# Performance work log

Hardware: AMD Instinct MI355X
Metric: run time of the kernel (lower is better)

## Reference

```python
import jax, jax.numpy as jnp
import numpy as np

N = 4096          # nodes
IN_DIM = 256
OUT_DIM = 128
EDGE_DIM = 64
N_SAMPLE = 128
N_EDGES = 65536   # undirected edges (edge ids 1..N_EDGES; id 0 = no edge)
ALPHA = 0.2       # leaky-relu negative slope


def _glorot(key, shape):
    fan_in, fan_out = shape[0], shape[-1]
    scale = 1.414 * np.sqrt(2.0 / (fan_in + fan_out))
    return jax.random.normal(key, shape, jnp.float32) * scale


def setup_inputs() -> dict:
    rng = np.random.default_rng(0)
    # sample unique undirected edges (i < j); np.unique sorts lexicographically,
    # which matches torch's row-major e_index.nonzero() ordering, so assigning
    # sequential ids 1..n here makes edges == arange(1, n+1) in the update step.
    ii = rng.integers(0, N, size=3 * N_EDGES)
    jj = rng.integers(0, N, size=3 * N_EDGES)
    lo, hi = np.minimum(ii, jj), np.maximum(ii, jj)
    ok = lo < hi
    pairs = np.unique(np.stack([lo[ok], hi[ok]], axis=1), axis=0)[:N_EDGES]
    n = pairs.shape[0]
    ids = np.arange(1, n + 1, dtype=np.int32)
    e_index = np.zeros((N, N), np.int32)
    e_index[pairs[:, 0], pairs[:, 1]] = ids
    e_index[pairs[:, 1], pairs[:, 0]] = ids
    # per-node neighbor sampling with replacement (hoisted from torch forward)
    neigh = np.empty((N, N_SAMPLE), np.int32)
    for v in range(N):
        nz = np.nonzero(e_index[v])[0]
        neigh[v] = v if nz.size == 0 else rng.choice(nz, N_SAMPLE)

    key = jax.random.key(0)
    ks = jax.random.split(key, 8)
    return {
        "features": jax.random.normal(ks[0], (N, IN_DIM), jnp.float32),
        "e_index": jnp.asarray(e_index),
        "neigh": jnp.asarray(neigh),
        "to_update": jnp.asarray(pairs.astype(np.int32)),
        "emb": jax.random.normal(ks[1], (n + 1, EDGE_DIM), jnp.float32),
        "W": _glorot(ks[2], (IN_DIM, OUT_DIM)),
        "W2": _glorot(ks[3], (OUT_DIM, EDGE_DIM)),
        "W3": _glorot(ks[4], (EDGE_DIM, EDGE_DIM)),
        "B": _glorot(ks[5], (1, EDGE_DIM)),
        "a": _glorot(ks[6], (2 * OUT_DIM + EDGE_DIM, 1)),
    }


def reference(features, e_index, neigh, to_update, emb, W, W2, W3, B, a):
    x = features @ W                                        # [N, OUT]
    xn = x[neigh]                                           # [N, S, OUT] gather
    eid = jnp.take_along_axis(e_index, neigh, axis=1)       # [N, S] edge ids
    en = emb[eid]                                           # [N, S, ED] gather
    a_input = jnp.concatenate(
        [jnp.broadcast_to(x[:, None, :], xn.shape), xn, en], axis=2
    )                                                       # [N, S, 2*OUT+ED]
    e = jax.nn.leaky_relu((a_input @ a)[..., 0], ALPHA)     # [N, S]
    att = jax.nn.softmax(e, axis=1)                         # dropout = id (eval)
    h_prime = jnp.einsum('ns,nsd->nd', att, xn)             # [N, OUT]
    output = jax.nn.elu(h_prime + x)
    # edge update: (output[i] + output[j]) @ W2 == matmul(output[pair], W2).sum(1)
    edges = e_index[to_update[:, 0], to_update[:, 1]]       # == 1..n
    v_input = (output[to_update[:, 0]] + output[to_update[:, 1]]) @ W2
    e_input = emb[edges] @ W3
    a_in2 = jnp.concatenate([B, e_input + v_input + B], axis=0)  # [n+1, ED]
    emb_new = jax.nn.relu(a_in2 * emb)
    return output, emb_new
```

## Files before the change

kernel.cpp:

```cpp
#include <hip/hip_runtime.h>
#include <hip/hip_bf16.h>

#define N_NODES 4096
#define IN_DIM  256
#define OUT_DIM 128
#define EDGE_DIM 64
#define N_SAMPLE 128

__device__ __forceinline__ float wsum64(float v) {
#pragma unroll
  for (int off = 32; off; off >>= 1) v += __shfl_xor(v, off, 64);
  return v;
}
__device__ __forceinline__ float sum16(float v) {
#pragma unroll
  for (int off = 1; off < 16; off <<= 1) v += __shfl_xor(v, off, 64);
  return v;
}
__device__ __forceinline__ float bfu(ushort u) {
  return __uint_as_float((unsigned int)u << 16);
}

__global__ void __launch_bounds__(128) k1_kernel(const float* __restrict__ feat,
                                                 const float* __restrict__ W,
                                                 const float* __restrict__ emb,
                                                 const int* __restrict__ eidx,
                                                 const int* __restrict__ neigh,
                                                 const float* __restrict__ a,
                                                 ushort* __restrict__ xh,
                                                 float* __restrict__ s1,
                                                 float* __restrict__ s2,
                                                 float* __restrict__ s3,
                                                 int* __restrict__ eid_vs, int rows) {
  const int t  = threadIdx.x;
  const int v0 = blockIdx.x * 4;
  __shared__ float f[4][IN_DIM];
  __shared__ float redA[8], redB[8];

  int uq[4];
#pragma unroll
  for (int q = 0; q < 4; ++q) uq[q] = neigh[(v0 + q) * N_SAMPLE + t];

  {
    float4* f4 = reinterpret_cast<float4*>(&f[0][0]);
    const float4* g4 = reinterpret_cast<const float4*>(&feat[v0 * IN_DIM]);
    f4[t]       = g4[t];
    f4[t + 128] = g4[t + 128];
  }
  __syncthreads();

  int eq[4];
#pragma unroll
  for (int q = 0; q < 4; ++q) eq[q] = eidx[(v0 + q) * N_NODES + uq[q]];

  float acc[4] = {0.f, 0.f, 0.f, 0.f};
#pragma unroll 2
  for (int i = 0; i < IN_DIM; i += 4) {
    const float w0 = W[(i + 0) * OUT_DIM + t];
    const float w1 = W[(i + 1) * OUT_DIM + t];
    const float w2 = W[(i + 2) * OUT_DIM + t];
    const float w3 = W[(i + 3) * OUT_DIM + t];
#pragma unroll
    for (int r = 0; r < 4; ++r) {
      const float4 fv = *reinterpret_cast<const float4*>(&f[r][i]);
      acc[r] += fv.x * w0 + fv.y * w1 + fv.z * w2 + fv.w * w3;
    }
  }

#pragma unroll
  for (int q = 0; q < 4; ++q) eid_vs[(v0 + q) * N_SAMPLE + t] = eq[q];

  const int wv = t >> 6;
  const float a1t = a[t], a2t = a[OUT_DIM + t];
#pragma unroll
  for (int r = 0; r < 4; ++r) {
    unsigned int ub = __float_as_uint(acc[r]);
    ub += 0x7FFFu + ((ub >> 16) & 1u);
    xh[(v0 + r) * OUT_DIM + t] = (ushort)(ub >> 16);
    const float q1 = wsum64(acc[r] * a1t);
    const float q2 = wsum64(acc[r] * a2t);
    if ((t & 63) == 0) { redA[wv * 4 + r] = q1; redB[wv * 4 + r] = q2; }
  }
  __syncthreads();
  if (t < 4) {
    s1[v0 + t] = redA[t] + redA[4 + t];
    s2[v0 + t] = redB[t] + redB[4 + t];
  }

  const int gw  = blockIdx.x * 2 + wv;
  const int l   = t & 63;
  const int sub = l >> 4, q16 = l & 15;
  const float4 a3q = *reinterpret_cast<const float4*>(&a[2 * OUT_DIM + q16 * 4]);
  for (int r0 = gw * 4; r0 < rows; r0 += 8192) {
    const int r = r0 + sub;
    float v = 0.f;
    if (r < rows) {
      const float4 e4 = *reinterpret_cast<const float4*>(&emb[r * EDGE_DIM + q16 * 4]);
      v = e4.x * a3q.x + e4.y * a3q.y + e4.z * a3q.z + e4.w * a3q.w;
    }
    v = sum16(v);
    if (q16 == 0 && r < rows) s3[r] = v;
  }
}

__global__ void __launch_bounds__(256, 4) k2_attn_y_kernel(const ushort* __restrict__ xh,
                                                           const float* __restrict__ s1,
                                                           const float* __restrict__ s2,
                                                           const float* __restrict__ s3,
                                                           const int* __restrict__ neigh,
                                                           const int* __restrict__ eid_vs,
                                                           const float* __restrict__ W2,
                                                           float* __restrict__ out,
                                                           float* __restrict__ Y) {
  const int v = blockIdx.x;
  const int t = threadIdx.x;
  const int w = t >> 6, l = t & 63;
  __shared__ float attC[N_SAMPLE];
  __shared__ float redC[2];
  __shared__ float4 hpC[8][32];
  __shared__ float orow[OUT_DIM];
  __shared__ float partY[4][EDGE_DIM];

  const int half = l >> 5, cq = l & 31;
  const int s0 = w * 32;
  ushort4 xr[16];
#pragma unroll
  for (int it = 0; it < 16; ++it) {
    const int u = neigh[v * N_SAMPLE + s0 + 2 * it + half];
    xr[it] = *reinterpret_cast<const ushort4*>(&xh[u * OUT_DIM + cq * 4]);
  }

  if (t < N_SAMPLE) {
    const int u   = neigh[v * N_SAMPLE + t];
    const int eid = eid_vs[v * N_SAMPLE + t];
    float e = s1[v] + s2[u] + s3[eid];
    e = e > 0.f ? e : 0.2f * e;
    const float p = __expf(e);
    attC[t] = p;
    const float s = wsum64(p);
    if (l == 0) redC[w] = s;
  }
  __syncthreads();
  const float inv = 1.0f / (redC[0] + redC[1]);

  {
    float4 h4 = make_float4(0.f, 0.f, 0.f, 0.f);
#pragma unroll
    for (int it = 0; it < 16; ++it) {
      const float av = attC[s0 + 2 * it + half];
      h4.x += av * bfu(xr[it].x);
      h4.y += av * bfu(xr[it].y);
      h4.z += av * bfu(xr[it].z);
      h4.w += av * bfu(xr[it].w);
    }
    hpC[w * 2 + half][cq] = h4;
  }
  __syncthreads();

  if (t < 32) {
    float4 H = make_float4(0.f, 0.f, 0.f, 0.f);
#pragma unroll
    for (int p = 0; p < 8; ++p) {
      const float4 v4 = hpC[p][t];
      H.x += v4.x; H.y += v4.y; H.z += v4.z; H.w += v4.w;
    }
    const ushort4 xs = *reinterpret_cast<const ushort4*>(&xh[v * OUT_DIM + t * 4]);
    float o0 = H.x * inv + bfu(xs.x), o1 = H.y * inv + bfu(xs.y);
    float o2 = H.z * inv + bfu(xs.z), o3 = H.w * inv + bfu(xs.w);
    o0 = o0 > 0.f ? o0 : expm1f(o0);
    o1 = o1 > 0.f ? o1 : expm1f(o1);
    o2 = o2 > 0.f ? o2 : expm1f(o2);
    o3 = o3 > 0.f ? o3 : expm1f(o3);
    const float4 r = make_float4(o0, o1, o2, o3);
    *reinterpret_cast<float4*>(&out[v * OUT_DIM + t * 4]) = r;
    *reinterpret_cast<float4*>(&orow[t * 4]) = r;
  }
  __syncthreads();

  {
    const int c = t & 63, ks = t >> 6;
    float acc = 0.f;
#pragma unroll 8
    for (int k = ks * 32; k < ks * 32 + 32; ++k)
      acc += orow[k] * W2[k * EDGE_DIM + c];
    partY[ks][c] = acc;
  }
  __syncthreads();
  if (t < EDGE_DIM)
    Y[v * EDGE_DIM + t] = partY[0][t] + partY[1][t] + partY[2][t] + partY[3][t];
}

#define TE 64
__global__ void __launch_bounds__(256) edge_fused_kernel(const float* __restrict__ Y,
                                                         const float* __restrict__ emb,
                                                         const int* __restrict__ eidx,
                                                         const int* __restrict__ tu,
                                                         const float* __restrict__ W3,
                                                         const float* __restrict__ Bv,
                                                         float* __restrict__ emb_new, int n) {
  const int t  = threadIdx.x;
  const int k0 = blockIdx.x * TE;
  __shared__ float Ain[TE][68];
  __shared__ int   tus[2 * TE];

  if (t < 2 * TE) {
    const int idx = 2 * k0 + t;
    tus[t] = (idx < 2 * n) ? tu[idx] : 0;
  }
  {
    const int e  = t >> 2, q = t & 3;
    const int ke = k0 + e;
    if (ke < n) {
      const int i = tu[2 * ke], j = tu[2 * ke + 1];
      const int id = eidx[i * N_NODES + j];
#pragma unroll
      for (int kk = 0; kk < 16; kk += 4) {
        const int k = q * 16 + kk;
        *reinterpret_cast<float4*>(&Ain[e][k]) =
            *reinterpret_cast<const float4*>(&emb[id * EDGE_DIM + k]);
      }
    }
  }
  __syncthreads();

  const int e0 = (t >> 4) * 4;
  const int c0 = (t & 15) * 4;
  const float4 b4 = *reinterpret_cast<const float4*>(&Bv[c0]);
  float4 acc[4];
#pragma unroll
  for (int m = 0; m < 4; ++m) acc[m] = b4;

#pragma unroll 4
  for (int k = 0; k < EDGE_DIM; k += 4) {
    float4 a4[4];
#pragma unroll
    for (int m = 0; m < 4; ++m) a4[m] = *reinterpret_cast<const float4*>(&Ain[e0 + m][k]);
#pragma unroll
    for (int kk = 0; kk < 4; ++kk) {
      const float4 wv = *reinterpret_cast<const float4*>(&W3[(k + kk) * EDGE_DIM + c0]);
#pragma unroll
      for (int m = 0; m < 4; ++m) {
        const float av = reinterpret_cast<const float*>(&a4[m])[kk];
        acc[m].x += av * wv.x; acc[m].y += av * wv.y;
        acc[m].z += av * wv.z; acc[m].w += av * wv.w;
      }
    }
  }

#pragma unroll
  for (int m = 0; m < 4; ++m) {
    const int ke = k0 + e0 + m;
    if (ke < n) {
      const int i = tus[2 * (e0 + m)], j = tus[2 * (e0 + m) + 1];
      const float4 yi = *reinterpret_cast<const float4*>(&Y[i * EDGE_DIM + c0]);
      const float4 yj = *reinterpret_cast<const float4*>(&Y[j * EDGE_DIM + c0]);
      const float4 ek = *reinterpret_cast<const float4*>(&emb[(ke + 1) * EDGE_DIM + c0]);
      float4 r;
      r.x = fmaxf((acc[m].x + yi.x + yj.x) * ek.x, 0.f);
      r.y = fmaxf((acc[m].y + yi.y + yj.y) * ek.y, 0.f);
      r.z = fmaxf((acc[m].z + yi.z + yj.z) * ek.z, 0.f);
      r.w = fmaxf((acc[m].w + yi.w + yj.w) * ek.w, 0.f);
      *reinterpret_cast<float4*>(&emb_new[(ke + 1) * EDGE_DIM + c0]) = r;
    }
  }
  if (blockIdx.x == 0 && t < 16) {
    const int cc = t * 4;
    const float4 b0 = *reinterpret_cast<const float4*>(&Bv[cc]);
    const float4 e0v = *reinterpret_cast<const float4*>(&emb[cc]);
    float4 r;
    r.x = fmaxf(b0.x * e0v.x, 0.f);
    r.y = fmaxf(b0.y * e0v.y, 0.f);
    r.z = fmaxf(b0.z * e0v.z, 0.f);
    r.w = fmaxf(b0.w * e0v.w, 0.f);
    *reinterpret_cast<float4*>(&emb_new[cc]) = r;
  }
}

extern "C" void kernel_launch(void* const* d_in, const int* in_sizes, int n_in,
                              void* d_out, int out_size, void* d_ws, size_t ws_size,
                              hipStream_t stream) {
  const float* feat  = (const float*)d_in[0];
  const int*   eidx  = (const int*)d_in[1];
  const int*   neigh = (const int*)d_in[2];
  const int*   tu    = (const int*)d_in[3];
  const float* emb   = (const float*)d_in[4];
  const float* W     = (const float*)d_in[5];
  const float* W2    = (const float*)d_in[6];
  const float* W3    = (const float*)d_in[7];
  const float* Bv    = (const float*)d_in[8];
  const float* a     = (const float*)d_in[9];
  const int n    = in_sizes[3] / 2;
  const int rows = in_sizes[4] / EDGE_DIM;

  float* ws = (float*)d_ws;
  float* s1     = ws + 524288;
  float* s2     = ws + 528384;
  float* s3     = ws + 532480;
  float* Y      = ws + 598032;
  ushort* xh    = (ushort*)(ws + 860176);
  int*  eid_vs  = (int*)(ws + 1122320);

  float* out_nodes = (float*)d_out;
  float* emb_new   = out_nodes + N_NODES * OUT_DIM;

  hipLaunchKernelGGL(k1_kernel, dim3(N_NODES / 4), dim3(128), 0, stream,
                     feat, W, emb, eidx, neigh, a, xh, s1, s2, s3, eid_vs, rows);
  hipLaunchKernelGGL(k2_attn_y_kernel, dim3(N_NODES), dim3(256), 0, stream,
                     xh, s1, s2, s3, neigh, eid_vs, W2, out_nodes, Y);
  hipLaunchKernelGGL(edge_fused_kernel, dim3((n + TE - 1) / TE), dim3(256), 0, stream,
                     Y, emb, eidx, tu, W3, Bv, emb_new, n);
}
```

Measured before the change: 176.6 us.

## Move edge emb@W3 GEMM into first kernel and split node GEMM across 256 threads

New measurement: 172.7 us. 2.2% less time.

```diff
diff --git a/kernel.cpp b/kernel.cpp
--- a/kernel.cpp
+++ b/kernel.cpp
@@ -21,65 +21,91 @@
   return __uint_as_float((unsigned int)u << 16);
 }
 
-__global__ void __launch_bounds__(128) k1_kernel(const float* __restrict__ feat,
+__global__ void __launch_bounds__(256) k1_kernel(const float* __restrict__ feat,
                                                  const float* __restrict__ W,
                                                  const float* __restrict__ emb,
                                                  const int* __restrict__ eidx,
                                                  const int* __restrict__ neigh,
+                                                 const int* __restrict__ tu,
                                                  const float* __restrict__ a,
+                                                 const float* __restrict__ W3,
+                                                 const float* __restrict__ Bv,
                                                  ushort* __restrict__ xh,
                                                  float* __restrict__ s1,
                                                  float* __restrict__ s2,
                                                  float* __restrict__ s3,
-                                                 int* __restrict__ eid_vs, int rows) {
-  const int t  = threadIdx.x;
-  const int v0 = blockIdx.x * 4;
-  __shared__ float f[4][IN_DIM];
+                                                 int* __restrict__ eid_vs,
+                                                 float* __restrict__ Z,
+                                                 int n, int rows) {
+  const int t   = threadIdx.x;
+  const int bid = blockIdx.x;
+  const int v0  = bid * 4;
+  const int k0z = bid * 64;
+  __shared__ float U[4352];
   __shared__ float redA[8], redB[8];
-
-  int uq[4];
-#pragma unroll
-  for (int q = 0; q < 4; ++q) uq[q] = neigh[(v0 + q) * N_SAMPLE + t];
-
+  __shared__ int   tusS[128];
+  __shared__ int   eidS[64];
+
+  if (t < 128) tusS[t] = (2 * k0z + t < 2 * n) ? tu[2 * k0z + t] : 0;
+  int uq[2];
+#pragma unroll
+  for (int q = 0; q < 2; ++q) {
+    const int idx = t + 256 * q, r = idx >> 7, s = idx & 127;
+    uq[q] = neigh[(v0 + r) * N_SAMPLE + s];
+  }
+  reinterpret_cast<float4*>(U)[t] =
+      reinterpret_cast<const float4*>(&feat[v0 * IN_DIM])[t];
+  __syncthreads();
+
+  int eq[2];
+#pragma unroll
+  for (int q = 0; q < 2; ++q) {
+    const int idx = t + 256 * q, r = idx >> 7;
+    eq[q] = eidx[(v0 + r) * N_NODES + uq[q]];
+  }
+  if (t < 64) {
+    const int ke = k0z + t;
+    eidS[t] = (ke < n) ? eidx[tusS[2 * t] * N_NODES + tusS[2 * t + 1]] : 0;
+  }
+
+  const int h = t >> 7, c = t & 127;
   {
-    float4* f4 = reinterpret_cast<float4*>(&f[0][0]);
-    const float4* g4 = reinterpret_cast<const float4*>(&feat[v0 * IN_DIM]);
-    f4[t]       = g4[t];
-    f4[t + 128] = g4[t + 128];
-  }
-  __syncthreads();
-
-  int eq[4];
-#pragma unroll
-  for (int q = 0; q < 4; ++q) eq[q] = eidx[(v0 + q) * N_NODES + uq[q]];
-
-  float acc[4] = {0.f, 0.f, 0.f, 0.f};
-#pragma unroll 2
-  for (int i = 0; i < IN_DIM; i += 4) {
-    const float w0 = W[(i + 0) * OUT_DIM + t];
-    const float w1 = W[(i + 1) * OUT_DIM + t];
-    const float w2 = W[(i + 2) * OUT_DIM + t];
-    const float w3 = W[(i + 3) * OUT_DIM + t];
+    float acc4[4] = {0.f, 0.f, 0.f, 0.f};
+    const int kb = h * 128;
+    for (int k = kb; k < kb + 128; k += 4) {
+      const float w0 = W[(k + 0) * OUT_DIM + c];
+      const float w1 = W[(k + 1) * OUT_DIM + c];
+      const float w2 = W[(k + 2) * OUT_DIM + c];
+      const float w3 = W[(k + 3) * OUT_DIM + c];
+#pragma unroll
+      for (int r = 0; r < 4; ++r) {
+        const float4 fv = *reinterpret_cast<const float4*>(&U[r * 256 + k]);
+        acc4[r] += fv.x * w0 + fv.y * w1 + fv.z * w2 + fv.w * w3;
+      }
+    }
+#pragma unroll
+    for (int r = 0; r < 4; ++r) U[1024 + (h * 4 + r) * 128 + c] = acc4[r];
+  }
+  __syncthreads();
+
+  if (t < 128) {
+    const float a1t = a[t], a2t = a[OUT_DIM + t];
+    const int wv = t >> 6;
 #pragma unroll
     for (int r = 0; r < 4; ++r) {
-      const float4 fv = *reinterpret_cast<const float4*>(&f[r][i]);
-      acc[r] += fv.x * w0 + fv.y * w1 + fv.z * w2 + fv.w * w3;
-    }
-  }
-
-#pragma unroll
-  for (int q = 0; q < 4; ++q) eid_vs[(v0 + q) * N_SAMPLE + t] = eq[q];
-
-  const int wv = t >> 6;
-  const float a1t = a[t], a2t = a[OUT_DIM + t];
-#pragma unroll
-  for (int r = 0; r < 4; ++r) {
-    unsigned int ub = __float_as_uint(acc[r]);
-    ub += 0x7FFFu + ((ub >> 16) & 1u);
-    xh[(v0 + r) * OUT_DIM + t] = (ushort)(ub >> 16);
-    const float q1 = wsum64(acc[r] * a1t);
-    const float q2 = wsum64(acc[r] * a2t);
-    if ((t & 63) == 0) { redA[wv * 4 + r] = q1; redB[wv * 4 + r] = q2; }
+      const float xv = U[1024 + r * 128 + t] + U[1024 + (4 + r) * 128 + t];
+      unsigned int ub = __float_as_uint(xv);
+      ub += 0x7FFFu + ((ub >> 16) & 1u);
+      xh[(v0 + r) * OUT_DIM + t] = (ushort)(ub >> 16);
+      const float q1 = wsum64(xv * a1t);
+      const float q2 = wsum64(xv * a2t);
+      if ((t & 63) == 0) { redA[wv * 4 + r] = q1; redB[wv * 4 + r] = q2; }
+    }
+  }
+#pragma unroll
+  for (int q = 0; q < 2; ++q) {
+    const int idx = t + 256 * q, r = idx >> 7, s = idx & 127;
+    eid_vs[(v0 + r) * N_SAMPLE + s] = eq[q];
   }
   __syncthreads();
   if (t < 4) {
@@ -87,19 +113,66 @@
     s2[v0 + t] = redB[t] + redB[4 + t];
   }
 
-  const int gw  = blockIdx.x * 2 + wv;
-  const int l   = t & 63;
-  const int sub = l >> 4, q16 = l & 15;
-  const float4 a3q = *reinterpret_cast<const float4*>(&a[2 * OUT_DIM + q16 * 4]);
-  for (int r0 = gw * 4; r0 < rows; r0 += 8192) {
-    const int r = r0 + sub;
-    float v = 0.f;
-    if (r < rows) {
-      const float4 e4 = *reinterpret_cast<const float4*>(&emb[r * EDGE_DIM + q16 * 4]);
-      v = e4.x * a3q.x + e4.y * a3q.y + e4.z * a3q.z + e4.w * a3q.w;
-    }
-    v = sum16(v);
-    if (q16 == 0 && r < rows) s3[r] = v;
+  {
+    const int wv = t >> 6, l = t & 63;
+    const int gw = bid * 4 + wv;
+    const int sub = l >> 4, q16 = l & 15;
+    const float4 a3q = *reinterpret_cast<const float4*>(&a[2 * OUT_DIM + q16 * 4]);
+    for (int r0 = gw * 4; r0 < rows; r0 += 16384) {
+      const int r = r0 + sub;
+      float v = 0.f;
+      if (r < rows) {
+        const float4 e4 = *reinterpret_cast<const float4*>(&emb[r * EDGE_DIM + q16 * 4]);
+        v = e4.x * a3q.x + e4.y * a3q.y + e4.z * a3q.z + e4.w * a3q.w;
+      }
+      v = sum16(v);
+      if (q16 == 0 && r < rows) s3[r] = v;
+    }
+  }
+  __syncthreads();
+
+  if (k0z < n) {
+    const int e = t >> 2, q = t & 3;
+    const int id = eidS[e];
+#pragma unroll
+    for (int kk = 0; kk < 16; kk += 4) {
+      const int k = q * 16 + kk;
+      *reinterpret_cast<float4*>(&U[e * 68 + k]) =
+          *reinterpret_cast<const float4*>(&emb[id * EDGE_DIM + k]);
+    }
+  }
+  __syncthreads();
+
+  if (k0z < n) {
+    const int e0 = (t >> 4) * 4;
+    const int c0 = (t & 15) * 4;
+    const float4 b4 = *reinterpret_cast<const float4*>(&Bv[c0]);
+    float4 acc[4];
+#pragma unroll
+    for (int m = 0; m < 4; ++m) acc[m] = b4;
+#pragma unroll 4
+    for (int k = 0; k < EDGE_DIM; k += 4) {
+      float4 a4[4];
+#pragma unroll
+      for (int m = 0; m < 4; ++m)
+        a4[m] = *reinterpret_cast<const float4*>(&U[(e0 + m) * 68 + k]);
+#pragma unroll
+      for (int kk = 0; kk < 4; ++kk) {
+        const float4 wv = *reinterpret_cast<const float4*>(&W3[(k + kk) * EDGE_DIM + c0]);
+#pragma unroll
+        for (int m = 0; m < 4; ++m) {
+          const float av = reinterpret_cast<const float*>(&a4[m])[kk];
+          acc[m].x += av * wv.x; acc[m].y += av * wv.y;
+          acc[m].z += av * wv.z; acc[m].w += av * wv.w;
+        }
+      }
+    }
+#pragma unroll
+    for (int m = 0; m < 4; ++m) {
+      const int ke = k0z + e0 + m;
+      if (ke < n)
+        *reinterpret_cast<float4*>(&Z[ke * EDGE_DIM + c0]) = acc[m];
+    }
   }
 }
 
@@ -190,76 +263,34 @@
     Y[v * EDGE_DIM + t] = partY[0][t] + partY[1][t] + partY[2][t] + partY[3][t];
 }
 
-#define TE 64
-__global__ void __launch_bounds__(256) edge_fused_kernel(const float* __restrict__ Y,
-                                                         const float* __restrict__ emb,
-                                                         const int* __restrict__ eidx,
-                                                         const int* __restrict__ tu,
-                                                         const float* __restrict__ W3,
-                                                         const float* __restrict__ Bv,
-                                                         float* __restrict__ emb_new, int n) {
+__global__ void __launch_bounds__(256) k3_kernel(const float* __restrict__ Z,
+                                                 const float* __restrict__ Y,
+                                                 const float* __restrict__ emb,
+                                                 const int* __restrict__ tu,
+                                                 const float* __restrict__ Bv,
+                                                 float* __restrict__ emb_new, int n) {
   const int t  = threadIdx.x;
-  const int k0 = blockIdx.x * TE;
-  __shared__ float Ain[TE][68];
-  __shared__ int   tus[2 * TE];
-
-  if (t < 2 * TE) {
-    const int idx = 2 * k0 + t;
-    tus[t] = (idx < 2 * n) ? tu[idx] : 0;
-  }
-  {
-    const int e  = t >> 2, q = t & 3;
-    const int ke = k0 + e;
-    if (ke < n) {
-      const int i = tu[2 * ke], j = tu[2 * ke + 1];
-      const int id = eidx[i * N_NODES + j];
-#pragma unroll
-      for (int kk = 0; kk < 16; kk += 4) {
-        const int k = q * 16 + kk;
-        *reinterpret_cast<float4*>(&Ain[e][k]) =
-            *reinterpret_cast<const float4*>(&emb[id * EDGE_DIM + k]);
-      }
-    }
-  }
+  const int k0 = blockIdx.x * 64;
+  __shared__ int tus[128];
+  if (t < 128) tus[t] = (2 * k0 + t < 2 * n) ? tu[2 * k0 + t] : 0;
   __syncthreads();
 
   const int e0 = (t >> 4) * 4;
   const int c0 = (t & 15) * 4;
-  const float4 b4 = *reinterpret_cast<const float4*>(&Bv[c0]);
-  float4 acc[4];
-#pragma unroll
-  for (int m = 0; m < 4; ++m) acc[m] = b4;
-
-#pragma unroll 4
-  for (int k = 0; k < EDGE_DIM; k += 4) {
-    float4 a4[4];
-#pragma unroll
-    for (int m = 0; m < 4; ++m) a4[m] = *reinterpret_cast<const float4*>(&Ain[e0 + m][k]);
-#pragma unroll
-    for (int kk = 0; kk < 4; ++kk) {
-      const float4 wv = *reinterpret_cast<const float4*>(&W3[(k + kk) * EDGE_DIM + c0]);
-#pragma unroll
-      for (int m = 0; m < 4; ++m) {
-        const float av = reinterpret_cast<const float*>(&a4[m])[kk];
-        acc[m].x += av * wv.x; acc[m].y += av * wv.y;
-        acc[m].z += av * wv.z; acc[m].w += av * wv.w;
-      }
-    }
-  }
-
 #pragma unroll
   for (int m = 0; m < 4; ++m) {
     const int ke = k0 + e0 + m;
     if (ke < n) {
       const int i = tus[2 * (e0 + m)], j = tus[2 * (e0 + m) + 1];
+      const float4 z4 = *reinterpret_cast<const float4*>(&Z[ke * EDGE_DIM + c0]);
       const float4 yi = *reinterpret_cast<const float4*>(&Y[i * EDGE_DIM + c0]);
       const float4 yj = *reinterpret_cast<const float4*>(&Y[j * EDGE_DIM + c0]);
       const float4 ek = *reinterpret_cast<const float4*>(&emb[(ke + 1) * EDGE_DIM + c0]);
       float4 r;
-      r.x = fmaxf((acc[m].x + yi.x + yj.x) * ek.x, 0.f);
-      r.y = fmaxf((acc[m].y + yi.y + yj.y) * ek.y, 0.f);
-      r.z = fmaxf((acc[m].z + yi.z + yj.z) * ek.z, 0.f);
-      r.w = fmaxf((acc[m].w + yi.w + yj.w) * ek.w, 0.f);
+      r.x = fmaxf((z4.x + yi.x + yj.x) * ek.x, 0.f);
+      r.y = fmaxf((z4.y + yi.y + yj.y) * ek.y, 0.f);
+      r.z = fmaxf((z4.z + yi.z + yj.z) * ek.z, 0.f);
+      r.w = fmaxf((z4.w + yi.w + yj.w) * ek.w, 0.f);
       *reinterpret_cast<float4*>(&emb_new[(ke + 1) * EDGE_DIM + c0]) = r;
     }
   }
@@ -299,14 +330,16 @@
   float* Y      = ws + 598032;
   ushort* xh    = (ushort*)(ws + 860176);
   int*  eid_vs  = (int*)(ws + 1122320);
+  float* Z      = ws + 1646608;
 
   float* out_nodes = (float*)d_out;
   float* emb_new   = out_nodes + N_NODES * OUT_DIM;
 
-  hipLaunchKernelGGL(k1_kernel, dim3(N_NODES / 4), dim3(128), 0, stream,
-                     feat, W, emb, eidx, neigh, a, xh, s1, s2, s3, eid_vs, rows);
+  hipLaunchKernelGGL(k1_kernel, dim3(N_NODES / 4), dim3(256), 0, stream,
+                     feat, W, emb, eidx, neigh, tu, a, W3, Bv,
+                     xh, s1, s2, s3, eid_vs, Z, n, rows);
   hipLaunchKernelGGL(k2_attn_y_kernel, dim3(N_NODES), dim3(256), 0, stream,
                      xh, s1, s2, s3, neigh, eid_vs, W2, out_nodes, Y);
-  hipLaunchKernelGGL(edge_fused_kernel, dim3((n + TE - 1) / TE), dim3(256), 0, stream,
-                     Y, emb, eidx, tu, W3, Bv, emb_new, n);
-}
+  hipLaunchKernelGGL(k3_kernel, dim3((n + 63) / 64), dim3(256), 0, stream,
+                     Z, Y, emb, tu, Bv, emb_new, n);
+}
```
